# Performance work log

Measured on AMD Instinct MI355X. Metric: run time of the kernel, lower is better.

Reference implementation:

```python
import jax, jax.numpy as jnp
import numpy as np

B, N, D = 2, 2048, 1024
H = 16
D_HEAD = D // H
WINDOW = 128


def setup_inputs() -> dict:
    key = jax.random.key(0)
    ks = jax.random.split(key, 9)
    s = 1.0 / np.sqrt(D)
    return {
        "x": jax.random.normal(ks[0], (B, N, D), dtype=jnp.float32),
        "Wq": jax.random.uniform(ks[1], (D, D), jnp.float32, -s, s),
        "bq": jax.random.uniform(ks[2], (D,), jnp.float32, -s, s),
        "Wk": jax.random.uniform(ks[3], (D, D), jnp.float32, -s, s),
        "bk": jax.random.uniform(ks[4], (D,), jnp.float32, -s, s),
        "Wv": jax.random.uniform(ks[5], (D, D), jnp.float32, -s, s),
        "bv": jax.random.uniform(ks[6], (D,), jnp.float32, -s, s),
        "Wo": jax.random.uniform(ks[7], (D, D), jnp.float32, -s, s),
        "bo": jax.random.uniform(ks[8], (D,), jnp.float32, -s, s),
    }


def reference(x, Wq, bq, Wk, bk, Wv, bv, Wo, bo):
    # Projections (torch Linear: x @ W.T + b), split into heads: (B,H,N,d)
    def proj(W, b):
        y = x @ W.T + b
        return y.reshape(B, N, H, D_HEAD).transpose(0, 2, 1, 3)

    Q = proj(Wq, bq)
    K = proj(Wk, bk)
    V = proj(Wv, bv)

    scale = 1.0 / np.sqrt(D_HEAD)
    scores = jnp.einsum("bhqd,bhkd->bhqk", Q, K) * scale  # (B,H,N,N)

    i = jnp.arange(N)[:, None]
    j = jnp.arange(N)[None, :]
    band = jnp.abs(i - j) <= WINDOW  # (N,N) sliding-window band mask
    scores = jnp.where(band, scores, -jnp.inf)

    probs = jax.nn.softmax(scores, axis=-1)
    out = jnp.einsum("bhqk,bhkd->bhqd", probs, V)  # (B,H,N,d)
    out = out.transpose(0, 2, 1, 3).reshape(B, N, D)
    return out @ Wo.T + bo
```

## Files before the change

### kernel.cpp

```cpp
#include <hip/hip_runtime.h>
#include <hip/hip_bf16.h>
#include <stdint.h>

typedef __bf16 bf16_t;
typedef __bf16 bf16x8 __attribute__((ext_vector_type(8)));
typedef float f32x4 __attribute__((ext_vector_type(4)));

#define NB 2
#define NN 2048
#define ND 1024
#define NH 16
#define DHEAD 64
#define WIN 128

__device__ __forceinline__ void load_lds16(const void* g, void* l) {
  __builtin_amdgcn_global_load_lds(
      (const __attribute__((address_space(1))) uint32_t*)g,
      (__attribute__((address_space(3))) uint32_t*)l, 16, 0, 0);
}

__global__ __launch_bounds__(256) void cast_kernel(const float* __restrict__ in,
                                                   bf16_t* __restrict__ out, int n4) {
  int i = blockIdx.x * 256 + threadIdx.x;
  if (i < n4) {
    float4 v = reinterpret_cast<const float4*>(in)[i];
    union { bf16_t h[4]; uint2 u; } o;
    o.h[0] = (bf16_t)v.x; o.h[1] = (bf16_t)v.y;
    o.h[2] = (bf16_t)v.z; o.h[3] = (bf16_t)v.w;
    reinterpret_cast<uint2*>(out)[i] = o.u;
  }
}

__global__ __launch_bounds__(256) void cast4_kernel(const float* __restrict__ i0, const float* __restrict__ i1,
                                                    const float* __restrict__ i2, const float* __restrict__ i3,
                                                    bf16_t* o0, bf16_t* o1, bf16_t* o2, bf16_t* o3, int n4) {
  int z = blockIdx.y;
  const float* in = (z == 0) ? i0 : (z == 1) ? i1 : (z == 2) ? i2 : i3;
  bf16_t* out = (z == 0) ? o0 : (z == 1) ? o1 : (z == 2) ? o2 : o3;
  int i = blockIdx.x * 256 + threadIdx.x;
  if (i < n4) {
    float4 v = reinterpret_cast<const float4*>(in)[i];
    union { bf16_t h[4]; uint2 u; } o;
    o.h[0] = (bf16_t)v.x; o.h[1] = (bf16_t)v.y;
    o.h[2] = (bf16_t)v.z; o.h[3] = (bf16_t)v.w;
    reinterpret_cast<uint2*>(out)[i] = o.u;
  }
}

__device__ __forceinline__ void gemm_tile(const bf16_t* __restrict__ A,
                                          const bf16_t* __restrict__ Bw,
                                          bf16_t* As, bf16_t* Bs,
                                          int m0, int n0, f32x4 acc[4][4]) {
  const int tid  = threadIdx.x;
  const int lane = tid & 63;
  const int wid  = tid >> 6;
  const int wr = wid >> 1, wc = wid & 1;
  const int lrow = lane & 15, lkg = lane >> 4;
  const int srow = lane >> 2, scol = (lane & 3) * 8;

  for (int k0 = 0; k0 < 1024; k0 += 32) {
#pragma unroll
    for (int i = 0; i < 2; ++i) {
      const int rbase = (wid * 2 + i) * 16;
      load_lds16(A  + (size_t)(m0 + rbase + srow) * 1024 + k0 + scol, As + rbase * 32);
      load_lds16(Bw + (size_t)(n0 + rbase + srow) * 1024 + k0 + scol, Bs + rbase * 32);
    }
    __syncthreads();
    bf16x8 af[4], bf[4];
#pragma unroll
    for (int m = 0; m < 4; ++m)
      af[m] = *reinterpret_cast<const bf16x8*>(As + (wr * 64 + m * 16 + lrow) * 32 + lkg * 8);
#pragma unroll
    for (int n = 0; n < 4; ++n)
      bf[n] = *reinterpret_cast<const bf16x8*>(Bs + (wc * 64 + n * 16 + lrow) * 32 + lkg * 8);
#pragma unroll
    for (int m = 0; m < 4; ++m)
#pragma unroll
      for (int n = 0; n < 4; ++n)
        acc[m][n] = __builtin_amdgcn_mfma_f32_16x16x32_bf16(af[m], bf[n], acc[m][n], 0, 0, 0);
    __syncthreads();
  }
}

__global__ __launch_bounds__(256, 2)
void qkv_gemm(const bf16_t* __restrict__ xb,
              const bf16_t* __restrict__ Wqb, const bf16_t* __restrict__ Wkb,
              const bf16_t* __restrict__ Wvb,
              const float* __restrict__ bq, const float* __restrict__ bk,
              const float* __restrict__ bv,
              bf16_t* __restrict__ Qh, bf16_t* __restrict__ Kh,
              bf16_t* __restrict__ VTt) {
  __shared__ __align__(16) bf16_t As[128 * 32];
  __shared__ __align__(16) bf16_t Bs[128 * 32];
  const int z = blockIdx.z;
  const bf16_t* Bw  = (z == 0) ? Wqb : (z == 1) ? Wkb : Wvb;
  const float* bias = (z == 0) ? bq  : (z == 1) ? bk  : bv;
  const int m0 = blockIdx.y * 128, n0 = blockIdx.x * 128;
  f32x4 acc[4][4] = {};
  gemm_tile(xb, Bw, As, Bs, m0, n0, acc);

  const int lane = threadIdx.x & 63;
  const int wid  = threadIdx.x >> 6;
  const int wr = wid >> 1, wc = wid & 1;
  const int lrow = lane & 15, lkg = lane >> 4;
#pragma unroll
  for (int m = 0; m < 4; ++m)
#pragma unroll
    for (int n = 0; n < 4; ++n)
#pragma unroll
      for (int r = 0; r < 4; ++r) {
        int row = m0 + wr * 64 + m * 16 + lkg * 4 + r;
        int col = n0 + wc * 64 + n * 16 + lrow;
        float val = acc[m][n][r] + bias[col];
        int bb = row >> 11, tok = row & 2047;
        int hh = col >> 6,  dd = col & 63;
        if (z == 2) {
          VTt[((((size_t)(bb * NH + hh) * 32 + (tok >> 6)) * 64 + dd) << 6) + (tok & 63)] = (bf16_t)val;
        } else {
          bf16_t* outp = (z == 0) ? Qh : Kh;
          outp[(((size_t)(bb * NH + hh) * NN + tok) << 6) + dd] = (bf16_t)val;
        }
      }
}

__global__ __launch_bounds__(256, 2)
void out_gemm(const bf16_t* __restrict__ AOb, const bf16_t* __restrict__ Wob,
              const float* __restrict__ bo, float* __restrict__ Cout) {
  __shared__ __align__(16) bf16_t As[128 * 32];
  __shared__ __align__(16) bf16_t Bs[128 * 32];
  const int m0 = blockIdx.y * 128, n0 = blockIdx.x * 128;
  f32x4 acc[4][4] = {};
  gemm_tile(AOb, Wob, As, Bs, m0, n0, acc);

  const int lane = threadIdx.x & 63;
  const int wid  = threadIdx.x >> 6;
  const int wr = wid >> 1, wc = wid & 1;
  const int lrow = lane & 15, lkg = lane >> 4;
#pragma unroll
  for (int m = 0; m < 4; ++m)
#pragma unroll
    for (int n = 0; n < 4; ++n)
#pragma unroll
      for (int r = 0; r < 4; ++r) {
        int row = m0 + wr * 64 + m * 16 + lkg * 4 + r;
        int col = n0 + wc * 64 + n * 16 + lrow;
        Cout[(size_t)row * 1024 + col] = acc[m][n][r] + bo[col];
      }
}

__global__ __launch_bounds__(256)
void attn_kernel(const bf16_t* __restrict__ Qh, const bf16_t* __restrict__ Kh,
                 const bf16_t* __restrict__ VTt, bf16_t* __restrict__ AO) {
  __shared__ __align__(16) bf16_t KV_lds[2][2][4096];
  __shared__ uint32_t P_lds[4][16][32];

  const int work = ((blockIdx.x & 7) << 7) | (blockIdx.x >> 3);
  const int qt = work & 31, h = (work >> 5) & 15, b = work >> 9;
  const int tid = threadIdx.x, lane = tid & 63, w = tid >> 6;
  const int lrow = lane & 15, lkg = lane >> 4;
  const int q0 = qt * 64;
  const int qb = q0 + w * 16;
  const int qrow = qb + lrow;
  const int rs7 = lrow & 7;

  const int srow8 = lane >> 3;
  const int sswz  = 8 * ((lane & 7) ^ srow8);

  const bf16_t* kbase = Kh  + ((size_t)(b * NH + h) * NN) * DHEAD;
  const bf16_t* vbase = VTt + ((size_t)(b * NH + h) * (NN / 64)) * DHEAD * 64;

  const bf16_t* qptr = Qh + (((size_t)(b * NH + h) * NN + qrow) << 6) + lkg * 8;
  bf16x8 qf0 = *reinterpret_cast<const bf16x8*>(qptr);
  bf16x8 qf1 = *reinterpret_cast<const bf16x8*>(qptr + 32);

  float m_run = -1e30f, l_run = 0.f;
  f32x4 o[4] = {};

  const int kstart = (q0 - WIN > 0) ? (q0 - WIN) : 0;
  const int kend = (q0 + 64 + WIN < NN) ? (q0 + 64 + WIN) : NN;
  const int nch = (kend - kstart) >> 6;
  const float scale = 0.125f;

  auto stage = [&](int bufi, int kc) {
#pragma unroll
    for (int j = 0; j < 2; ++j) {
      const int i = w * 2 + j;
      load_lds16(kbase + (((size_t)(kc + i * 8 + srow8)) << 6) + sswz,
                 &KV_lds[bufi][0][i * 512]);
      load_lds16(vbase + (((size_t)((kc >> 6) * 64 + i * 8 + srow8)) << 6) + sswz,
                 &KV_lds[bufi][1][i * 512]);
    }
  };

  stage(0, kstart);
  __syncthreads();

  for (int ic = 0; ic < nch; ++ic) {
    const int kc = kstart + ic * 64;
    const int bi = ic & 1;
    if (ic + 1 < nch) stage(bi ^ 1, kc + 64);

    const bf16_t* Kt = &KV_lds[bi][0][0];
    const bf16_t* Vt = &KV_lds[bi][1][0];

    f32x4 s[4];
#pragma unroll
    for (int t = 0; t < 4; ++t) {
      const bf16_t* kr = Kt + (t * 16 + lrow) * 64;
      bf16x8 kf0 = *reinterpret_cast<const bf16x8*>(kr + ((lkg ^ rs7) << 3));
      bf16x8 kf1 = *reinterpret_cast<const bf16x8*>(kr + (((4 + lkg) ^ rs7) << 3));
      f32x4 zz = {};
      zz = __builtin_amdgcn_mfma_f32_16x16x32_bf16(kf0, qf0, zz, 0, 0, 0);
      zz = __builtin_amdgcn_mfma_f32_16x16x32_bf16(kf1, qf1, zz, 0, 0, 0);
      s[t] = zz;
    }

    bf16x8 vf0[4], vf1[4];
#pragma unroll
    for (int f = 0; f < 4; ++f) {
      const bf16_t* vr = Vt + (f * 16 + lrow) * 64;
      vf0[f] = *reinterpret_cast<const bf16x8*>(vr + ((lkg ^ rs7) << 3));
      vf1[f] = *reinterpret_cast<const bf16x8*>(vr + (((4 + lkg) ^ rs7) << 3));
    }

    const bool needs_mask = (kc < qb - 113) || (kc > qb + 65);
    float p[4][4];
    float mloc = -1e30f, rsum = 0.f;
    if (needs_mask) {
      float v[4][4];
#pragma unroll
      for (int t = 0; t < 4; ++t)
#pragma unroll
        for (int r = 0; r < 4; ++r) {
          int k = kc + t * 16 + lkg * 4 + r;
          int d = qrow - k;
          bool ok = (unsigned)(d + WIN) <= 2u * WIN;
          v[t][r] = ok ? s[t][r] * scale : -1e30f;
          mloc = fmaxf(mloc, v[t][r]);
        }
      mloc = fmaxf(mloc, __shfl_xor(mloc, 16, 64));
      mloc = fmaxf(mloc, __shfl_xor(mloc, 32, 64));
      float mn = fmaxf(m_run, mloc);
      float corr = __expf(m_run - mn);
      m_run = mn;
#pragma unroll
      for (int t = 0; t < 4; ++t)
#pragma unroll
        for (int r = 0; r < 4; ++r) {
          int k = kc + t * 16 + lkg * 4 + r;
          int d = qrow - k;
          bool ok = (unsigned)(d + WIN) <= 2u * WIN;
          p[t][r] = ok ? __expf(v[t][r] - mn) : 0.f;
          rsum += p[t][r];
        }
      rsum += __shfl_xor(rsum, 16, 64);
      rsum += __shfl_xor(rsum, 32, 64);
      l_run = l_run * corr + rsum;
#pragma unroll
      for (int f = 0; f < 4; ++f) o[f] *= corr;
    } else {
      float v[4][4];
#pragma unroll
      for (int t = 0; t < 4; ++t)
#pragma unroll
        for (int r = 0; r < 4; ++r) {
          v[t][r] = s[t][r] * scale;
          mloc = fmaxf(mloc, v[t][r]);
        }
      mloc = fmaxf(mloc, __shfl_xor(mloc, 16, 64));
      mloc = fmaxf(mloc, __shfl_xor(mloc, 32, 64));
      float mn = fmaxf(m_run, mloc);
      float corr = __expf(m_run - mn);
      m_run = mn;
#pragma unroll
      for (int t = 0; t < 4; ++t)
#pragma unroll
        for (int r = 0; r < 4; ++r) {
          p[t][r] = __expf(v[t][r] - mn);
          rsum += p[t][r];
        }
      rsum += __shfl_xor(rsum, 16, 64);
      rsum += __shfl_xor(rsum, 32, 64);
      l_run = l_run * corr + rsum;
#pragma unroll
      for (int f = 0; f < 4; ++f) o[f] *= corr;
    }

    uint32_t* prow = &P_lds[w][lrow][0];
#pragma unroll
    for (int t = 0; t < 4; ++t)
#pragma unroll
      for (int c = 0; c < 2; ++c) {
        union { bf16_t hh[2]; uint32_t u; } pk;
        pk.hh[0] = (bf16_t)p[t][2 * c];
        pk.hh[1] = (bf16_t)p[t][2 * c + 1];
        int L = 8 * t + 2 * lkg + c;
        int pos = (((L >> 2) ^ rs7) << 2) | (L & 3);
        prow[pos] = pk.u;
      }
    asm volatile("" ::: "memory");
    const bf16_t* prd = reinterpret_cast<const bf16_t*>(&P_lds[w][lrow][0]);
    bf16x8 pa0 = *reinterpret_cast<const bf16x8*>(prd + ((lkg ^ rs7) << 3));
    bf16x8 pa1 = *reinterpret_cast<const bf16x8*>(prd + (((4 + lkg) ^ rs7) << 3));

#pragma unroll
    for (int f = 0; f < 4; ++f) {
      o[f] = __builtin_amdgcn_mfma_f32_16x16x32_bf16(vf0[f], pa0, o[f], 0, 0, 0);
      o[f] = __builtin_amdgcn_mfma_f32_16x16x32_bf16(vf1[f], pa1, o[f], 0, 0, 0);
    }
    __syncthreads();
  }

  float inv = 1.0f / l_run;
#pragma unroll
  for (int f = 0; f < 4; ++f) {
    union { bf16_t hh[4]; uint2 u; } ov;
#pragma unroll
    for (int r = 0; r < 4; ++r) ov.hh[r] = (bf16_t)(o[f][r] * inv);
    bf16_t* op = AO + (size_t)(b * NN + qrow) * ND + h * DHEAD + f * 16 + lkg * 4;
    *reinterpret_cast<uint2*>(op) = ov.u;
  }
}

extern "C" void kernel_launch(void* const* d_in, const int* in_sizes, int n_in,
                              void* d_out, int out_size, void* d_ws, size_t ws_size,
                              hipStream_t stream) {
  const float* x  = (const float*)d_in[0];
  const float* Wq = (const float*)d_in[1];
  const float* bq = (const float*)d_in[2];
  const float* Wk = (const float*)d_in[3];
  const float* bk = (const float*)d_in[4];
  const float* Wv = (const float*)d_in[5];
  const float* bv = (const float*)d_in[6];
  const float* Wo = (const float*)d_in[7];
  const float* bo = (const float*)d_in[8];
  float* out = (float*)d_out;

  bf16_t* ws  = (bf16_t*)d_ws;
  bf16_t* xb  = ws;
  bf16_t* Wqb = xb  + 4194304;
  bf16_t* Wkb = Wqb + 1048576;
  bf16_t* Wvb = Wkb + 1048576;
  bf16_t* Wob = Wvb + 1048576;
  bf16_t* Qh  = Wob + 1048576;
  bf16_t* Kh  = Qh  + 4194304;
  bf16_t* VTt = Kh  + 4194304;
  bf16_t* AOb = VTt + 4194304;

  cast_kernel<<<4096, 256, 0, stream>>>(x, xb, 1048576);
  cast4_kernel<<<dim3(1024, 4), 256, 0, stream>>>(Wq, Wk, Wv, Wo, Wqb, Wkb, Wvb, Wob, 262144);

  qkv_gemm<<<dim3(8, 32, 3), 256, 0, stream>>>(xb, Wqb, Wkb, Wvb, bq, bk, bv, Qh, Kh, VTt);
  attn_kernel<<<1024, 256, 0, stream>>>(Qh, Kh, VTt, AOb);
  out_gemm<<<dim3(8, 32), 256, 0, stream>>>(AOb, Wob, bo, out);
}
```

Measured before the change: 96.20 us.

## Rewrite QKV GEMM with 8-wave 128x256 tiles and triple-buffered LDS pipeline

Replaces the QKV projection GEMM with a 512-thread kernel that computes 128x256 output tiles. It streams K-slices through a three-stage LDS ring using async global-to-LDS loads and a partial vmcnt wait, so loads overlap the MFMA work. It also adds an XOR swizzle to cut LDS bank conflicts, a block-index swizzle for L2 locality, and setprio around the MFMA section. The cost is more LDS and higher register pressure per block, and the manual waitcnt and barrier choreography is fragile.

After: 103.9 us. +8.0%, slower.

```diff
diff --git a/kernel.cpp b/kernel.cpp
--- a/kernel.cpp
+++ b/kernel.cpp
@@ -47,6 +47,99 @@
   }
 }
 
+__global__ __launch_bounds__(512, 4)
+void qkv_gemm8(const bf16_t* __restrict__ xb,
+               const bf16_t* __restrict__ Wqb, const bf16_t* __restrict__ Wkb,
+               const bf16_t* __restrict__ Wvb,
+               const float* __restrict__ bq, const float* __restrict__ bk,
+               const float* __restrict__ bv,
+               bf16_t* __restrict__ Qh, bf16_t* __restrict__ Kh,
+               bf16_t* __restrict__ VTt) {
+  __shared__ __align__(16) bf16_t lds[3][12288];
+
+  const int raw = blockIdx.x;
+  const int swz = (raw & 7) * 48 + (raw >> 3);
+  const int mt = swz / 12, nt = swz % 12;
+  const int m0 = mt * 128;
+  const int z = nt >> 2;
+  const int n0z = (nt & 3) * 256;
+  const bf16_t* Bw  = (z == 0) ? Wqb : (z == 1) ? Wkb : Wvb;
+  const float* bias = (z == 0) ? bq  : (z == 1) ? bk  : bv;
+
+  const int tid = threadIdx.x, lane = tid & 63, w = tid >> 6;
+  const int wm = w >> 2, wn = w & 3;
+  const int lrow = lane & 15, lkg = lane >> 4;
+  const int srow = lane >> 2;
+  const int schunk = (lane & 3) ^ (srow & 3);
+
+  const bf16_t* asrc  = xb + (size_t)(m0 + w * 16 + srow) * 1024 + schunk * 8;
+  const bf16_t* bsrc0 = Bw + (size_t)(n0z + (w * 2) * 16 + srow) * 1024 + schunk * 8;
+  const bf16_t* bsrc1 = bsrc0 + 16 * 1024;
+
+  f32x4 acc[4][4] = {};
+
+  auto stage = [&](int t) {
+    const int tt = (t < 32) ? t : (t - 32);
+    const int k0 = tt << 5;
+    bf16_t* buf = &lds[t % 3][0];
+    load_lds16(asrc + k0,  buf + w * 512);
+    load_lds16(bsrc0 + k0, buf + 4096 + (w * 2) * 512);
+    load_lds16(bsrc1 + k0, buf + 4096 + (w * 2 + 1) * 512);
+  };
+
+  stage(0);
+  stage(1);
+  asm volatile("s_waitcnt vmcnt(3)" ::: "memory");
+  __builtin_amdgcn_s_barrier();
+
+  for (int t = 0; t < 32; ++t) {
+    const bf16_t* Abuf = &lds[t % 3][0];
+    const bf16_t* Bbuf = Abuf + 4096;
+    bf16x8 af[4], bf[4];
+#pragma unroll
+    for (int m = 0; m < 4; ++m) {
+      const int row = wm * 64 + m * 16 + lrow;
+      af[m] = *reinterpret_cast<const bf16x8*>(Abuf + row * 32 + ((lkg ^ (row & 3)) << 3));
+    }
+#pragma unroll
+    for (int n = 0; n < 4; ++n) {
+      const int row = wn * 64 + n * 16 + lrow;
+      bf[n] = *reinterpret_cast<const bf16x8*>(Bbuf + row * 32 + ((lkg ^ (row & 3)) << 3));
+    }
+    stage(t + 2);
+    __builtin_amdgcn_s_barrier();
+    __builtin_amdgcn_s_setprio(1);
+#pragma unroll
+    for (int m = 0; m < 4; ++m)
+#pragma unroll
+      for (int n = 0; n < 4; ++n)
+        acc[m][n] = __builtin_amdgcn_mfma_f32_16x16x32_bf16(af[m], bf[n], acc[m][n], 0, 0, 0);
+    __builtin_amdgcn_s_setprio(0);
+    asm volatile("s_waitcnt vmcnt(3)" ::: "memory");
+    __builtin_amdgcn_s_barrier();
+    __builtin_amdgcn_sched_barrier(0);
+  }
+
+#pragma unroll
+  for (int m = 0; m < 4; ++m)
+#pragma unroll
+    for (int n = 0; n < 4; ++n)
+#pragma unroll
+      for (int r = 0; r < 4; ++r) {
+        const int grow = m0 + wm * 64 + m * 16 + lkg * 4 + r;
+        const int colz = n0z + wn * 64 + n * 16 + lrow;
+        float val = acc[m][n][r] + bias[colz];
+        const int bb = grow >> 11, tok = grow & 2047;
+        const int hh = colz >> 6, dd = colz & 63;
+        if (z == 2) {
+          VTt[((((size_t)(bb * NH + hh) * 32 + (tok >> 6)) * 64 + dd) << 6) + (tok & 63)] = (bf16_t)val;
+        } else {
+          bf16_t* outp = (z == 0) ? Qh : Kh;
+          outp[(((size_t)(bb * NH + hh) * NN + tok) << 6) + dd] = (bf16_t)val;
+        }
+      }
+}
+
 __device__ __forceinline__ void gemm_tile(const bf16_t* __restrict__ A,
                                           const bf16_t* __restrict__ Bw,
                                           bf16_t* As, bf16_t* Bs,
@@ -80,47 +173,6 @@
         acc[m][n] = __builtin_amdgcn_mfma_f32_16x16x32_bf16(af[m], bf[n], acc[m][n], 0, 0, 0);
     __syncthreads();
   }
-}
-
-__global__ __launch_bounds__(256, 2)
-void qkv_gemm(const bf16_t* __restrict__ xb,
-              const bf16_t* __restrict__ Wqb, const bf16_t* __restrict__ Wkb,
-              const bf16_t* __restrict__ Wvb,
-              const float* __restrict__ bq, const float* __restrict__ bk,
-              const float* __restrict__ bv,
-              bf16_t* __restrict__ Qh, bf16_t* __restrict__ Kh,
-              bf16_t* __restrict__ VTt) {
-  __shared__ __align__(16) bf16_t As[128 * 32];
-  __shared__ __align__(16) bf16_t Bs[128 * 32];
-  const int z = blockIdx.z;
-  const bf16_t* Bw  = (z == 0) ? Wqb : (z == 1) ? Wkb : Wvb;
-  const float* bias = (z == 0) ? bq  : (z == 1) ? bk  : bv;
-  const int m0 = blockIdx.y * 128, n0 = blockIdx.x * 128;
-  f32x4 acc[4][4] = {};
-  gemm_tile(xb, Bw, As, Bs, m0, n0, acc);
-
-  const int lane = threadIdx.x & 63;
-  const int wid  = threadIdx.x >> 6;
-  const int wr = wid >> 1, wc = wid & 1;
-  const int lrow = lane & 15, lkg = lane >> 4;
-#pragma unroll
-  for (int m = 0; m < 4; ++m)
-#pragma unroll
-    for (int n = 0; n < 4; ++n)
-#pragma unroll
-      for (int r = 0; r < 4; ++r) {
-        int row = m0 + wr * 64 + m * 16 + lkg * 4 + r;
-        int col = n0 + wc * 64 + n * 16 + lrow;
-        float val = acc[m][n][r] + bias[col];
-        int bb = row >> 11, tok = row & 2047;
-        int hh = col >> 6,  dd = col & 63;
-        if (z == 2) {
-          VTt[((((size_t)(bb * NH + hh) * 32 + (tok >> 6)) * 64 + dd) << 6) + (tok & 63)] = (bf16_t)val;
-        } else {
-          bf16_t* outp = (z == 0) ? Qh : Kh;
-          outp[(((size_t)(bb * NH + hh) * NN + tok) << 6) + dd] = (bf16_t)val;
-        }
-      }
 }
 
 __global__ __launch_bounds__(256, 2)
@@ -350,7 +402,7 @@
   cast_kernel<<<4096, 256, 0, stream>>>(x, xb, 1048576);
   cast4_kernel<<<dim3(1024, 4), 256, 0, stream>>>(Wq, Wk, Wv, Wo, Wqb, Wkb, Wvb, Wob, 262144);
 
-  qkv_gemm<<<dim3(8, 32, 3), 256, 0, stream>>>(xb, Wqb, Wkb, Wvb, bq, bk, bv, Qh, Kh, VTt);
+  qkv_gemm8<<<384, 512, 0, stream>>>(xb, Wqb, Wkb, Wvb, bq, bk, bv, Qh, Kh, VTt);
   attn_kernel<<<1024, 256, 0, stream>>>(Qh, Kh, VTt, AOb);
   out_gemm<<<dim3(8, 32), 256, 0, stream>>>(AOb, Wob, bo, out);
 }
```

## Double-buffer LDS in GEMM tiles and merge cast kernels into one launch

Applied to the files above, without the earlier changes.

The shared GEMM tile loop now uses two LDS buffers, issuing the global-to-LDS load for the next K slice before computing on the current one, so load latency can overlap MFMA work. The two fp32-to-bf16 cast kernels are merged into a single launch covering x and all four weight matrices, removing one kernel launch. LDS use per block doubles to 32 KB, which may affect occupancy. The loop keeps one barrier per iteration, so whether the prefetch write can collide with reads of the other buffer depends on the barrier placement in the unseen tail of the loop.

After: 97.12 us. Within noise of the previous version (+1.0%).

```diff
diff --git a/kernel.cpp b/kernel.cpp
--- a/kernel.cpp
+++ b/kernel.cpp
@@ -19,38 +19,37 @@
       (__attribute__((address_space(3))) uint32_t*)l, 16, 0, 0);
 }
 
-__global__ __launch_bounds__(256) void cast_kernel(const float* __restrict__ in,
-                                                   bf16_t* __restrict__ out, int n4) {
+__global__ __launch_bounds__(256)
+void cast_all(const float* __restrict__ x,
+              const float* __restrict__ Wq, const float* __restrict__ Wk,
+              const float* __restrict__ Wv, const float* __restrict__ Wo,
+              bf16_t* __restrict__ xb,
+              bf16_t* __restrict__ Wqb, bf16_t* __restrict__ Wkb,
+              bf16_t* __restrict__ Wvb, bf16_t* __restrict__ Wob) {
   int i = blockIdx.x * 256 + threadIdx.x;
-  if (i < n4) {
-    float4 v = reinterpret_cast<const float4*>(in)[i];
-    union { bf16_t h[4]; uint2 u; } o;
-    o.h[0] = (bf16_t)v.x; o.h[1] = (bf16_t)v.y;
-    o.h[2] = (bf16_t)v.z; o.h[3] = (bf16_t)v.w;
-    reinterpret_cast<uint2*>(out)[i] = o.u;
+  const float* in;
+  bf16_t* out;
+  int off;
+  if (i < 1048576) {
+    in = x; out = xb; off = i;
+  } else {
+    int j = i - 1048576;
+    int wsel = j >> 18;
+    off = j & 262143;
+    in  = (wsel == 0) ? Wq  : (wsel == 1) ? Wk  : (wsel == 2) ? Wv  : Wo;
+    out = (wsel == 0) ? Wqb : (wsel == 1) ? Wkb : (wsel == 2) ? Wvb : Wob;
   }
-}
-
-__global__ __launch_bounds__(256) void cast4_kernel(const float* __restrict__ i0, const float* __restrict__ i1,
-                                                    const float* __restrict__ i2, const float* __restrict__ i3,
-                                                    bf16_t* o0, bf16_t* o1, bf16_t* o2, bf16_t* o3, int n4) {
-  int z = blockIdx.y;
-  const float* in = (z == 0) ? i0 : (z == 1) ? i1 : (z == 2) ? i2 : i3;
-  bf16_t* out = (z == 0) ? o0 : (z == 1) ? o1 : (z == 2) ? o2 : o3;
-  int i = blockIdx.x * 256 + threadIdx.x;
-  if (i < n4) {
-    float4 v = reinterpret_cast<const float4*>(in)[i];
-    union { bf16_t h[4]; uint2 u; } o;
-    o.h[0] = (bf16_t)v.x; o.h[1] = (bf16_t)v.y;
-    o.h[2] = (bf16_t)v.z; o.h[3] = (bf16_t)v.w;
-    reinterpret_cast<uint2*>(out)[i] = o.u;
-  }
-}
-
-__device__ __forceinline__ void gemm_tile(const bf16_t* __restrict__ A,
-                                          const bf16_t* __restrict__ Bw,
-                                          bf16_t* As, bf16_t* Bs,
-                                          int m0, int n0, f32x4 acc[4][4]) {
+  float4 v = reinterpret_cast<const float4*>(in)[off];
+  union { bf16_t h[4]; uint2 u; } o;
+  o.h[0] = (bf16_t)v.x; o.h[1] = (bf16_t)v.y;
+  o.h[2] = (bf16_t)v.z; o.h[3] = (bf16_t)v.w;
+  reinterpret_cast<uint2*>(out)[off] = o.u;
+}
+
+__device__ __forceinline__ void gemm_tile_db(const bf16_t* __restrict__ A,
+                                             const bf16_t* __restrict__ Bw,
+                                             bf16_t* As, bf16_t* Bs,
+                                             int m0, int n0, f32x4 acc[4][4]) {
   const int tid  = threadIdx.x;
   const int lane = tid & 63;
   const int wid  = tid >> 6;
@@ -58,21 +57,32 @@
   const int lrow = lane & 15, lkg = lane >> 4;
   const int srow = lane >> 2, scol = (lane & 3) * 8;
 
-  for (int k0 = 0; k0 < 1024; k0 += 32) {
+  const bf16_t* abase = A  + (size_t)(m0 + srow) * 1024 + scol;
+  const bf16_t* bbase = Bw + (size_t)(n0 + srow) * 1024 + scol;
+
+  auto stage = [&](int buf, int k0) {
 #pragma unroll
     for (int i = 0; i < 2; ++i) {
       const int rbase = (wid * 2 + i) * 16;
-      load_lds16(A  + (size_t)(m0 + rbase + srow) * 1024 + k0 + scol, As + rbase * 32);
-      load_lds16(Bw + (size_t)(n0 + rbase + srow) * 1024 + k0 + scol, Bs + rbase * 32);
-    }
-    __syncthreads();
+      load_lds16(abase + (size_t)rbase * 1024 + k0, As + buf * 4096 + rbase * 32);
+      load_lds16(bbase + (size_t)rbase * 1024 + k0, Bs + buf * 4096 + rbase * 32);
+    }
+  };
+
+  stage(0, 0);
+  __syncthreads();
+
+  for (int t = 0; t < 32; ++t) {
+    if (t < 31) stage((t + 1) & 1, (t + 1) << 5);
+    const bf16_t* Ab = As + (t & 1) * 4096;
+    const bf16_t* Bb = Bs + (t & 1) * 4096;
     bf16x8 af[4], bf[4];
 #pragma unroll
     for (int m = 0; m < 4; ++m)
-      af[m] = *reinterpret_cast<const bf16x8*>(As + (wr * 64 + m * 16 + lrow) * 32 + lkg * 8);
+      af[m] = *reinterpret_cast<const bf16x8*>(Ab + (wr * 64 + m * 16 + lrow) * 32 + lkg * 8);
 #pragma unroll
     for (int n = 0; n < 4; ++n)
-      bf[n] = *reinterpret_cast<const bf16x8*>(Bs + (wc * 64 + n * 16 + lrow) * 32 + lkg * 8);
+      bf[n] = *reinterpret_cast<const bf16x8*>(Bb + (wc * 64 + n * 16 + lrow) * 32 + lkg * 8);
 #pragma unroll
     for (int m = 0; m < 4; ++m)
 #pragma unroll
@@ -90,14 +100,14 @@
               const float* __restrict__ bv,
               bf16_t* __restrict__ Qh, bf16_t* __restrict__ Kh,
               bf16_t* __restrict__ VTt) {
-  __shared__ __align__(16) bf16_t As[128 * 32];
-  __shared__ __align__(16) bf16_t Bs[128 * 32];
+  __shared__ __align__(16) bf16_t As[2 * 4096];
+  __shared__ __align__(16) bf16_t Bs[2 * 4096];
   const int z = blockIdx.z;
   const bf16_t* Bw  = (z == 0) ? Wqb : (z == 1) ? Wkb : Wvb;
   const float* bias = (z == 0) ? bq  : (z == 1) ? bk  : bv;
   const int m0 = blockIdx.y * 128, n0 = blockIdx.x * 128;
   f32x4 acc[4][4] = {};
-  gemm_tile(xb, Bw, As, Bs, m0, n0, acc);
+  gemm_tile_db(xb, Bw, As, Bs, m0, n0, acc);
 
   const int lane = threadIdx.x & 63;
   const int wid  = threadIdx.x >> 6;
@@ -126,11 +136,11 @@
 __global__ __launch_bounds__(256, 2)
 void out_gemm(const bf16_t* __restrict__ AOb, const bf16_t* __restrict__ Wob,
               const float* __restrict__ bo, float* __restrict__ Cout) {
-  __shared__ __align__(16) bf16_t As[128 * 32];
-  __shared__ __align__(16) bf16_t Bs[128 * 32];
+  __shared__ __align__(16) bf16_t As[2 * 4096];
+  __shared__ __align__(16) bf16_t Bs[2 * 4096];
   const int m0 = blockIdx.y * 128, n0 = blockIdx.x * 128;
   f32x4 acc[4][4] = {};
-  gemm_tile(AOb, Wob, As, Bs, m0, n0, acc);
+  gemm_tile_db(AOb, Wob, As, Bs, m0, n0, acc);
 
   const int lane = threadIdx.x & 63;
   const int wid  = threadIdx.x >> 6;
@@ -347,8 +357,7 @@
   bf16_t* VTt = Kh  + 4194304;
   bf16_t* AOb = VTt + 4194304;
 
-  cast_kernel<<<4096, 256, 0, stream>>>(x, xb, 1048576);
-  cast4_kernel<<<dim3(1024, 4), 256, 0, stream>>>(Wq, Wk, Wv, Wo, Wqb, Wkb, Wvb, Wob, 262144);
+  cast_all<<<8192, 256, 0, stream>>>(x, Wq, Wk, Wv, Wo, xb, Wqb, Wkb, Wvb, Wob);
 
   qkv_gemm<<<dim3(8, 32, 3), 256, 0, stream>>>(xb, Wqb, Wkb, Wvb, bq, bk, bv, Qh, Kh, VTt);
   attn_kernel<<<1024, 256, 0, stream>>>(Qh, Kh, VTt, AOb);
```
